# Kernel tuning notes

Measured on AMD Instinct MI355X. Metric: run time of the kernel, lower is better.

## Reference

```python
import jax, jax.numpy as jnp
import numpy as np

B, N, K, D, H, PQ, PV = 2, 2048, 30, 128, 4, 8, 4
INV3C = float(np.sqrt(1.0 / (3 * D)))      # 1/sqrt(3*hidden_dim)
INV3 = float(np.sqrt(1.0 / 3.0))
PT_SCALE = float(np.sqrt(1.0 / (3 * (PQ * 9.0 / 2))))


def _gather(nodes, idx):
    # nodes [B,N,...], idx [B,N,K] -> [B,N,K,...]
    return jax.vmap(lambda n, i: n[i])(nodes, idx)


def _ln(x, w, b, eps=1e-5):
    mu = x.mean(-1, keepdims=True)
    var = x.var(-1, keepdims=True)
    return (x - mu) / jnp.sqrt(var + eps) * w + b


def _forward(h_V, h_E, E_idx, R, t, mask_attend, mask_V,
             Wq, bq, Wkv, bkv, Wqp, bqp, Wkvp, bkvp, Wb, bb_, head_weights,
             Wout, bout, ln0_w, ln0_b, ln1_w, ln1_b, Wm1, bm1, Wm2, bm2):
    q = (h_V @ Wq + bq).reshape(B, N, H, D)                     # [B,N,H,C]
    kv = (h_V @ Wkv + bkv).reshape(B, N, H, 2 * D)
    k_, v_ = kv[..., :D], kv[..., D:]

    def apply_rigid(pts):  # pts [B,N,P,3] -> R @ p + t
        return jnp.einsum('bnxy,bnpy->bnpx', R, pts) + t[:, :, None, :]

    # torch builds points by split-into-3-then-stack along last dim
    qp = h_V @ Wqp + bqp                                        # [B,N,H*PQ*3]
    q_pts = jnp.stack(jnp.split(qp, 3, axis=-1), axis=-1)       # [B,N,H*PQ,3]
    q_pts = apply_rigid(q_pts).reshape(B, N, H, PQ, 3)
    kvp = h_V @ Wkvp + bkvp
    kv_pts = jnp.stack(jnp.split(kvp, 3, axis=-1), axis=-1)
    kv_pts = apply_rigid(kv_pts).reshape(B, N, H, PQ + PV, 3)
    k_pts, v_pts = kv_pts[..., :PQ, :], kv_pts[..., PQ:, :]

    b_bias = h_E @ Wb + bb_                                     # [B,N,K,H]
    k_nb = _gather(k_, E_idx)                                   # [B,N,K,H,C]
    a = jnp.einsum('bnhc,bnkhc->bnkh', q, k_nb) * INV3C
    a = a + INV3 * b_bias

    kp_nb = _gather(k_pts, E_idx)                               # [B,N,K,H,PQ,3]
    diff = q_pts[:, :, None] - kp_nb
    pt_att = jnp.sum(diff * diff, axis=-1)                      # [B,N,K,H,PQ]
    hw = jax.nn.softplus(head_weights)                          # [H]
    pt_att = jnp.sum(PT_SCALE * hw[None, None, None, :, None] * pt_att, axis=-1) * -0.5

    att_mask = 100000.0 * (mask_attend - 1.0)                   # [B,N,K]
    a = a + pt_att + att_mask[..., None]
    a = jax.nn.softmax(a, axis=-2)                              # softmax over neighbors K

    v_nb = _gather(v_, E_idx)
    o = jnp.einsum('bnkh,bnkhc->bnhc', a, v_nb).reshape(B, N, H * D)
    vp_nb = _gather(v_pts, E_idx)                               # [B,N,K,H,PV,3]
    o_pt = jnp.einsum('bnkh,bnkhpx->bnhpx', a, vp_nb)
    # invert_apply: R^T (x - t)
    o_pt = jnp.einsum('bnyx,bnhpy->bnhpx', R, o_pt - t[:, :, None, None, :])
    o_pt_norm = jnp.sqrt(jnp.sum(o_pt ** 2, axis=-1) + 1e-8).reshape(B, N, H * PV)
    o_pt = o_pt.reshape(B, N, H * PV, 3)
    o_pair = jnp.einsum('bnkh,bnkc->bnhc', a, h_E).reshape(B, N, H * D)

    cat = jnp.concatenate([o, o_pt[..., 0], o_pt[..., 1], o_pt[..., 2], o_pt_norm, o_pair], axis=-1)
    s = cat @ Wout + bout

    hv = _ln(h_V + s, ln0_w, ln0_b)
    m = jax.nn.relu(hv @ Wm1 + bm1) @ Wm2 + bm2
    hv = _ln(hv + m, ln1_w, ln1_b)
    return hv * mask_V[..., None]


def setup_inputs() -> dict:
    key = jax.random.key(0)
    ks = jax.random.split(key, 16)

    def dense(k, fi, fo):
        kw, kb = jax.random.split(k)
        s = 1.0 / np.sqrt(fi)
        return (jax.random.uniform(kw, (fi, fo), jnp.float32, -s, s),
                jax.random.uniform(kb, (fo,), jnp.float32, -s, s))

    h_V = jax.random.normal(ks[0], (B, N, D), jnp.float32)
    h_E = jax.random.normal(ks[1], (B, N, K, D), jnp.float32)
    E_idx = jax.random.randint(ks[2], (B, N, K), 0, N)
    Rr = jax.random.normal(ks[3], (B, N, 3, 3), jnp.float32)
    R, _ = jnp.linalg.qr(Rr)  # proper orthonormal frames
    t = jax.random.normal(ks[4], (B, N, 3), jnp.float32)
    mask_attend = jnp.ones((B, N, K), jnp.float32)
    mask_V = jnp.ones((B, N), jnp.float32)

    Wq, bq = dense(ks[5], D, D * H)
    Wkv, bkv = dense(ks[6], D, 2 * D * H)
    Wqp, bqp = dense(ks[7], D, H * PQ * 3)
    Wkvp, bkvp = dense(ks[8], D, H * (PQ + PV) * 3)
    Wb, bb_ = dense(ks[9], D, H)
    head_weights = jnp.full((H,), 0.541324854612918, jnp.float32)
    out_dim = H * (D + D + 4 * PV)
    Wout, bout = dense(ks[10], out_dim, D)
    ln0_w = jnp.ones((D,), jnp.float32); ln0_b = jnp.zeros((D,), jnp.float32)
    ln1_w = jnp.ones((D,), jnp.float32); ln1_b = jnp.zeros((D,), jnp.float32)
    Wm1, bm1 = dense(ks[11], D, 4 * D)
    Wm2, bm2 = dense(ks[12], 4 * D, D)
    return dict(h_V=h_V, h_E=h_E, E_idx=E_idx, R=R, t=t,
                mask_attend=mask_attend, mask_V=mask_V,
                Wq=Wq, bq=bq, Wkv=Wkv, bkv=bkv, Wqp=Wqp, bqp=bqp,
                Wkvp=Wkvp, bkvp=bkvp, Wb=Wb, bb_=bb_, head_weights=head_weights,
                Wout=Wout, bout=bout, ln0_w=ln0_w, ln0_b=ln0_b,
                ln1_w=ln1_w, ln1_b=ln1_b, Wm1=Wm1, bm1=bm1, Wm2=Wm2, bm2=bm2)


def reference(h_V, h_E, E_idx, R, t, mask_attend, mask_V,
              Wq, bq, Wkv, bkv, Wqp, bqp, Wkvp, bkvp, Wb, bb_, head_weights,
              Wout, bout, ln0_w, ln0_b, ln1_w, ln1_b, Wm1, bm1, Wm2, bm2):
    return _forward(h_V, h_E, E_idx, R, t, mask_attend, mask_V,
                    Wq, bq, Wkv, bkv, Wqp, bqp, Wkvp, bkvp, Wb, bb_, head_weights,
                    Wout, bout, ln0_w, ln0_b, ln1_w, ln1_b, Wm1, bm1, Wm2, bm2)
```

## Files before the change

kernel.cpp:

```cpp
#include <hip/hip_runtime.h>
#include <math.h>

#define BB 2
#define NN 2048
#define KK 30
#define DD 128
#define HH 4
#define PQ_ 8
#define PV_ 4
#define TM 16

#define INV3C    0.05103103630798288f
#define INV3     0.5773502691896258f
#define PT_SCALE 0.09622504486493764f

typedef __attribute__((ext_vector_type(8))) short short8;
typedef __attribute__((ext_vector_type(4))) float f32x4;
typedef unsigned short ushort_t;

__device__ __forceinline__ ushort_t f2bf(float f) {
    unsigned u = __float_as_uint(f);
    unsigned r = u + 0x7FFFu + ((u >> 16) & 1u);
    return (ushort_t)(r >> 16);
}
__device__ __forceinline__ float bf2f(ushort_t u) {
    return __uint_as_float(((unsigned)u) << 16);
}
__device__ __forceinline__ float bflo(unsigned u) {
    return __uint_as_float(u << 16);
}
__device__ __forceinline__ float bfhi(unsigned u) {
    return __uint_as_float(u & 0xffff0000u);
}

__global__ __launch_bounds__(256) void prep_kernel(
    const float* __restrict__ Wout, const float* __restrict__ Wm1,
    const float* __restrict__ Wm2,
    const float* __restrict__ Wq, const float* __restrict__ Wkv,
    const float* __restrict__ Wqp, const float* __restrict__ Wkvp,
    ushort_t* __restrict__ WoutT, ushort_t* __restrict__ Wm1T,
    ushort_t* __restrict__ Wm2T, ushort_t* __restrict__ WprojT)
{
    const int stride = gridDim.x * blockDim.x;
    const int t0 = blockIdx.x * blockDim.x + threadIdx.x;
    for (int idx = t0; idx < 128 * 1088; idx += stride) {
        int n = idx / 1088, k = idx - n * 1088;
        WoutT[idx] = f2bf(Wout[(size_t)k * 128 + n]);
    }
    for (int idx = t0; idx < 512 * 128; idx += stride) {
        int n = idx >> 7, k = idx & 127;
        Wm1T[idx] = f2bf(Wm1[(size_t)k * 512 + n]);
    }
    for (int idx = t0; idx < 128 * 512; idx += stride) {
        int n = idx >> 9, k = idx & 511;
        Wm2T[idx] = f2bf(Wm2[(size_t)k * 128 + n]);
    }
    for (int idx = t0; idx < 1792 * 128; idx += stride) {
        int n = idx >> 7, k = idx & 127;
        float v;
        if (n < 512)       v = Wq[(size_t)k * 512 + n];
        else if (n < 1536) v = Wkv[(size_t)k * 1024 + (n - 512)];
        else if (n < 1632) v = Wqp[k * 96 + (n - 1536)];
        else if (n < 1776) v = Wkvp[k * 144 + (n - 1632)];
        else               v = 0.f;
        WprojT[idx] = f2bf(v);
    }
}

__global__ __launch_bounds__(512) void proj_kernel(
    const float* __restrict__ hV, const float* __restrict__ R, const float* __restrict__ tvec,
    const ushort_t* __restrict__ WT,
    const float* __restrict__ bq, const float* __restrict__ bkv,
    const float* __restrict__ bqp, const float* __restrict__ bkvp,
    ushort_t* __restrict__ qb, ushort_t* __restrict__ kb, ushort_t* __restrict__ vb,
    float* __restrict__ qpts, float* __restrict__ kpts, float* __restrict__ vpts)
{
    const int node0 = (blockIdx.x >> 1) * TM;
    const int half  = blockIdx.x & 1;
    const int tid = threadIdx.x;
    const int w = tid >> 6, l = tid & 63, lr = l & 15, lk = l >> 4;

    __shared__ ushort_t s_A[TM][128];
    __shared__ float s_qp[TM][96];
    __shared__ float s_kvp[TM][144];

    {
        int i = tid * 4; int r = i >> 7, c = i & 127;
        float4 x = *(const float4*)&hV[(size_t)(node0 + r) * DD + c];
        s_A[r][c + 0] = f2bf(x.x); s_A[r][c + 1] = f2bf(x.y);
        s_A[r][c + 2] = f2bf(x.z); s_A[r][c + 3] = f2bf(x.w);
    }
    __syncthreads();

    const ushort_t* Ab = &s_A[lr][lk * 8];
    for (int t = 0; t < 7; ++t) {
        const int tile = half * 56 + w * 7 + t;
        const int n = tile * 16 + lr;
        f32x4 acc = {0.f, 0.f, 0.f, 0.f};
        const ushort_t* Bb = WT + (size_t)n * 128 + lk * 8;
        #pragma unroll
        for (int ks = 0; ks < 4; ++ks) {
            short8 a = *(const short8*)(Ab + ks * 32);
            short8 bfr = *(const short8*)(Bb + ks * 32);
            acc = __builtin_amdgcn_mfma_f32_16x16x32_bf16(a, bfr, acc, 0, 0, 0);
        }
        if (n < 512) {
            float bias = bq[n];
            #pragma unroll
            for (int i = 0; i < 4; ++i)
                qb[(size_t)(node0 + lk * 4 + i) * 512 + n] = f2bf(acc[i] + bias);
        } else if (n < 1536) {
            int n2 = n - 512;
            float bias = bkv[n2];
            int hh = n2 >> 8, wcol = n2 & 255;
            ushort_t* base = (wcol < 128) ? kb : vb;
            int off = hh * DD + (wcol & 127);
            #pragma unroll
            for (int i = 0; i < 4; ++i)
                base[(size_t)(node0 + lk * 4 + i) * 512 + off] = f2bf(acc[i] + bias);
        } else if (n < 1632) {
            int c = n - 1536;
            float bias = bqp[c];
            #pragma unroll
            for (int i = 0; i < 4; ++i) s_qp[lk * 4 + i][c] = acc[i] + bias;
        } else if (n < 1776) {
            int c = n - 1632;
            float bias = bkvp[c];
            #pragma unroll
            for (int i = 0; i < 4; ++i) s_kvp[lk * 4 + i][c] = acc[i] + bias;
        }
    }
    __syncthreads();

    if (half == 1) {
        for (int idx = tid; idx < TM * 96; idx += 512) {
            int r = idx / 96, u = idx % 96;
            int j = u / 3, d = u % 3;
            int node = node0 + r;
            float acc = tvec[node * 3 + d];
            #pragma unroll
            for (int y = 0; y < 3; ++y)
                acc = fmaf(R[node * 9 + d * 3 + y], s_qp[r][y * 32 + j], acc);
            qpts[(size_t)node * 96 + j * 3 + d] = acc;
        }
        for (int idx = tid; idx < TM * 144; idx += 512) {
            int r = idx / 144, u = idx % 144;
            int jj = u / 3, d = u % 3;
            int node = node0 + r;
            float acc = tvec[node * 3 + d];
            #pragma unroll
            for (int y = 0; y < 3; ++y)
                acc = fmaf(R[node * 9 + d * 3 + y], s_kvp[r][y * 48 + jj], acc);
            int hh = jj / 12, pp = jj % 12;
            if (pp < PQ_) kpts[(size_t)node * 96 + (hh * PQ_ + pp) * 3 + d] = acc;
            else          vpts[(size_t)node * 48 + (hh * PV_ + (pp - PQ_)) * 3 + d] = acc;
        }
    }
}

__global__ __launch_bounds__(256, 8) void attn_kernel(
    const float* __restrict__ hE, const int* __restrict__ Eidx,
    const float* __restrict__ R, const float* __restrict__ tvec,
    const float* __restrict__ mask_att,
    const float* __restrict__ Wb, const float* __restrict__ bb,
    const float* __restrict__ head_w,
    const ushort_t* __restrict__ qb, const ushort_t* __restrict__ kb,
    const ushort_t* __restrict__ vb,
    const float* __restrict__ qpts, const float* __restrict__ kpts, const float* __restrict__ vpts,
    ushort_t* __restrict__ catb)
{
    const int node = blockIdx.x;
    const int b = node >> 11;
    const int tid = threadIdx.x;
    const int lane = tid & 63;
    const int wv = tid >> 6;

    __shared__ ushort_t s_hEb[KK * DD];
    __shared__ float s_cat[1088];
    __shared__ float s_qp[96];
    __shared__ float s_p[HH][32];
    __shared__ int   s_j[32];
    __shared__ float s_mask[32];
    __shared__ float s_opt[48];

    if (tid < 96) s_qp[tid] = qpts[(size_t)node * 96 + tid];
    if (tid < KK) {
        s_j[tid] = Eidx[(size_t)node * KK + tid];
        s_mask[tid] = 100000.0f * (mask_att[(size_t)node * KK + tid] - 1.0f);
    }
    {
        const float4* src = (const float4*)(hE + (size_t)node * (KK * DD));
        #pragma unroll
        for (int i = 0; i < 4; ++i) {
            const int idx = tid + i * 256;
            if (idx < 960) {
                float4 x = src[idx];
                unsigned lo = ((unsigned)f2bf(x.y) << 16) | (unsigned)f2bf(x.x);
                unsigned hi = ((unsigned)f2bf(x.w) << 16) | (unsigned)f2bf(x.z);
                *(unsigned*)&s_hEb[idx * 4]     = lo;
                *(unsigned*)&s_hEb[idx * 4 + 2] = hi;
            }
        }
    }
    __syncthreads();

    const int h = wv;
    const int l32 = lane & 31;
    const int g = lane >> 5;

    const unsigned qu0 = *(const unsigned*)&qb[(size_t)node * 512 + h * DD + 2 * l32];
    const unsigned qu1 = *(const unsigned*)&qb[(size_t)node * 512 + h * DD + 64 + 2 * l32];
    const float q0 = bflo(qu0), q1 = bfhi(qu0), q2 = bflo(qu1), q3 = bfhi(qu1);
    const float wb0 = Wb[(2 * l32 +  0) * HH + h];
    const float wb1 = Wb[(2 * l32 +  1) * HH + h];
    const float wb2 = Wb[(2 * l32 + 64) * HH + h];
    const float wb3 = Wb[(2 * l32 + 65) * HH + h];
    const float cpt = -0.5f * PT_SCALE * log1pf(expf(head_w[h]));
    const float bbh = INV3 * bb[h];
    const float qpl = (l32 < 24) ? s_qp[h * 24 + l32] : 0.f;

    #pragma unroll
    for (int kx2 = 0; kx2 < KK / 2; ++kx2) {
        const int k = kx2 * 2 + g;
        size_t jb = (size_t)(b * NN + s_j[k]);
        const ushort_t* kr = kb + jb * 512 + h * DD;
        unsigned ku0 = *(const unsigned*)&kr[2 * l32];
        unsigned ku1 = *(const unsigned*)&kr[64 + 2 * l32];
        unsigned eu0 = *(const unsigned*)&s_hEb[k * DD + 2 * l32];
        unsigned eu1 = *(const unsigned*)&s_hEb[k * DD + 64 + 2 * l32];
        float s = q0 * bflo(ku0) + q1 * bfhi(ku0) + q2 * bflo(ku1) + q3 * bfhi(ku1);
        float t = wb0 * bflo(eu0) + wb1 * bfhi(eu0) + wb2 * bflo(eu1) + wb3 * bfhi(eu1);
        float ptc = 0.f;
        if (l32 < 24) {
            float d = qpl - kpts[jb * 96 + h * 24 + l32];
            ptc = d * d;
        }
        float val = INV3C * s + INV3 * t + cpt * ptc;
        #pragma unroll
        for (int off = 16; off; off >>= 1) val += __shfl_down(val, off, 32);
        if (l32 == 0) s_p[h][k] = val + bbh + s_mask[k];
    }
    __syncthreads();

    {
        float v = (lane < KK) ? s_p[h][lane] : -INFINITY;
        float m = v;
        #pragma unroll
        for (int off = 16; off; off >>= 1) m = fmaxf(m, __shfl_down(m, off));
        m = __shfl(m, 0);
        float e = (lane < KK) ? expf(v - m) : 0.f;
        float s = e;
        #pragma unroll
        for (int off = 16; off; off >>= 1) s += __shfl_down(s, off);
        s = __shfl(s, 0);
        if (lane < KK) s_p[h][lane] = e / s;
    }
    __syncthreads();

    {
        const int oh = tid >> 6;
        const int oc0 = (tid & 63) * 2;
        const ushort_t* vrow = vb + oh * DD + oc0;
        float a0 = 0.f, a1 = 0.f, b0 = 0.f, b1 = 0.f;
        #pragma unroll
        for (int kx = 0; kx < KK; ++kx) {
            unsigned pv = *(const unsigned*)(vrow + (size_t)(b * NN + s_j[kx]) * 512);
            unsigned pe = *(const unsigned*)&s_hEb[kx * DD + oc0];
            float p = s_p[oh][kx];
            a0 = fmaf(p, bflo(pv), a0);
            a1 = fmaf(p, bfhi(pv), a1);
            b0 = fmaf(p, bflo(pe), b0);
            b1 = fmaf(p, bfhi(pe), b1);
        }
        s_cat[oh * DD + oc0]           = a0;
        s_cat[oh * DD + oc0 + 1]       = a1;
        s_cat[576 + oh * DD + oc0]     = b0;
        s_cat[576 + oh * DD + oc0 + 1] = b1;
    }
    if (tid < 48) {
        const int oh = (tid / 3) >> 2;
        float acc = 0.f;
        #pragma unroll
        for (int kx = 0; kx < KK; ++kx)
            acc = fmaf(s_p[oh][kx], vpts[(size_t)(b * NN + s_j[kx]) * 48 + tid], acc);
        s_opt[tid] = acc;
    }
    __syncthreads();
    if (tid < 16) {
        int jj = tid;
        float g0 = s_opt[jj * 3 + 0] - tvec[node * 3 + 0];
        float g1 = s_opt[jj * 3 + 1] - tvec[node * 3 + 1];
        float g2 = s_opt[jj * 3 + 2] - tvec[node * 3 + 2];
        float l0 = R[node * 9 + 0] * g0 + R[node * 9 + 3] * g1 + R[node * 9 + 6] * g2;
        float l1 = R[node * 9 + 1] * g0 + R[node * 9 + 4] * g1 + R[node * 9 + 7] * g2;
        float l2 = R[node * 9 + 2] * g0 + R[node * 9 + 5] * g1 + R[node * 9 + 8] * g2;
        s_cat[512 + 0 * 16 + jj] = l0;
        s_cat[512 + 1 * 16 + jj] = l1;
        s_cat[512 + 2 * 16 + jj] = l2;
        s_cat[560 + jj] = sqrtf(l0 * l0 + l1 * l1 + l2 * l2 + 1e-8f);
    }
    __syncthreads();

    for (int i = tid; i < 1088; i += 256)
        catb[(size_t)node * 1088 + i] = f2bf(s_cat[i]);
}

__global__ __launch_bounds__(512) void tail_kernel(
    const float* __restrict__ hV, const float* __restrict__ maskV,
    const ushort_t* __restrict__ catb,
    const ushort_t* __restrict__ WoutT, const float* __restrict__ bout,
    const float* __restrict__ ln0w, const float* __restrict__ ln0b,
    const float* __restrict__ ln1w, const float* __restrict__ ln1b,
    const ushort_t* __restrict__ Wm1T, const float* __restrict__ bm1,
    const ushort_t* __restrict__ Wm2T, const float* __restrict__ bm2,
    float* __restrict__ out)
{
    const int node0 = blockIdx.x * TM;
    const int tid = threadIdx.x;
    const int w  = tid >> 6;
    const int l  = tid & 63;
    const int lr = l & 15;
    const int lk = l >> 4;

    __shared__ float    s_x[TM][DD];
    __shared__ float    s_hv[TM][DD];
    __shared__ ushort_t s_hvb[TM][136];
    __shared__ ushort_t s_m1[TM][520];
    __shared__ float    s_rs[TM][16];
    __shared__ float    s_rq[TM][16];
    __shared__ float    s_stat[TM][2];

    {
        f32x4 acc = {0.f, 0.f, 0.f, 0.f};
        const ushort_t* Ab = catb + (size_t)(node0 + lr) * 1088 + lk * 8;
        const ushort_t* Bb = WoutT + (size_t)(w * 16 + lr) * 1088 + lk * 8;
        #pragma unroll 2
        for (int ks = 0; ks < 34; ++ks) {
            short8 a = *(const short8*)(Ab + ks * 32);
            short8 bfr = *(const short8*)(Bb + ks * 32);
            acc = __builtin_amdgcn_mfma_f32_16x16x32_bf16(a, bfr, acc, 0, 0, 0);
        }
        #pragma unroll
        for (int i = 0; i < 4; ++i)
            s_x[lk * 4 + i][w * 16 + lr] = acc[i];
    }
    __syncthreads();

    if (tid < 256) {
        int r = tid >> 4, sg = tid & 15;
        float ss = 0.f, sq = 0.f;
        #pragma unroll
        for (int j = 0; j < 8; ++j) {
            int cc = sg * 8 + j;
            float x = s_x[r][cc] + bout[cc] + hV[(size_t)(node0 + r) * DD + cc];
            s_x[r][cc] = x;
            ss += x; sq += x * x;
        }
        s_rs[r][sg] = ss; s_rq[r][sg] = sq;
    }
    __syncthreads();
    if (tid < TM) {
        float ss = 0.f, sq = 0.f;
        #pragma unroll
        for (int sg = 0; sg < 16; ++sg) { ss += s_rs[tid][sg]; sq += s_rq[tid][sg]; }
        float mu = ss / 128.f;
        s_stat[tid][0] = mu;
        s_stat[tid][1] = rsqrtf(sq / 128.f - mu * mu + 1e-5f);
    }
    __syncthreads();
    {
        int idx = tid * 4;
        int r = idx >> 7, cc = idx & 127;
        float mu = s_stat[r][0], rstd = s_stat[r][1];
        #pragma unroll
        for (int j = 0; j < 4; ++j) {
            float hvv = (s_x[r][cc + j] - mu) * rstd * ln0w[cc + j] + ln0b[cc + j];
            s_hv[r][cc + j] = hvv;
            s_hvb[r][cc + j] = f2bf(hvv);
        }
    }
    __syncthreads();

    {
        const ushort_t* Ab = &s_hvb[lr][lk * 8];
        #pragma unroll
        for (int t = 0; t < 4; ++t) {
            int n0 = w * 64 + t * 16;
            f32x4 acc = {0.f, 0.f, 0.f, 0.f};
            const ushort_t* Bb = Wm1T + (size_t)(n0 + lr) * 128 + lk * 8;
            #pragma unroll
            for (int ks = 0; ks < 4; ++ks) {
                short8 a = *(const short8*)(Ab + ks * 32);
                short8 bfr = *(const short8*)(Bb + ks * 32);
                acc = __builtin_amdgcn_mfma_f32_16x16x32_bf16(a, bfr, acc, 0, 0, 0);
            }
            int n = n0 + lr;
            float bm = bm1[n];
            #pragma unroll
            for (int i = 0; i < 4; ++i)
                s_m1[lk * 4 + i][n] = f2bf(fmaxf(acc[i] + bm, 0.f));
        }
    }
    __syncthreads();

    {
        f32x4 acc = {0.f, 0.f, 0.f, 0.f};
        const ushort_t* Ab = &s_m1[lr][lk * 8];
        const ushort_t* Bb = Wm2T + (size_t)(w * 16 + lr) * 512 + lk * 8;
        #pragma unroll 4
        for (int ks = 0; ks < 16; ++ks) {
            short8 a = *(const short8*)(Ab + ks * 32);
            short8 bfr = *(const short8*)(Bb + ks * 32);
            acc = __builtin_amdgcn_mfma_f32_16x16x32_bf16(a, bfr, acc, 0, 0, 0);
        }
        #pragma unroll
        for (int i = 0; i < 4; ++i)
            s_x[lk * 4 + i][w * 16 + lr] = acc[i];
    }
    __syncthreads();

    if (tid < 256) {
        int r = tid >> 4, sg = tid & 15;
        float ss = 0.f, sq = 0.f;
        #pragma unroll
        for (int j = 0; j < 8; ++j) {
            int cc = sg * 8 + j;
            float x = s_x[r][cc] + bm2[cc] + s_hv[r][cc];
            s_x[r][cc] = x;
            ss += x; sq += x * x;
        }
        s_rs[r][sg] = ss; s_rq[r][sg] = sq;
    }
    __syncthreads();
    if (tid < TM) {
        float ss = 0.f, sq = 0.f;
        #pragma unroll
        for (int sg = 0; sg < 16; ++sg) { ss += s_rs[tid][sg]; sq += s_rq[tid][sg]; }
        float mu = ss / 128.f;
        s_stat[tid][0] = mu;
        s_stat[tid][1] = rsqrtf(sq / 128.f - mu * mu + 1e-5f);
    }
    __syncthreads();
    {
        int idx = tid * 4;
        int r = idx >> 7, cc = idx & 127;
        float mu = s_stat[r][0], rstd = s_stat[r][1];
        float mk = maskV[node0 + r];
        float4 o;
        o.x = ((s_x[r][cc + 0] - mu) * rstd * ln1w[cc + 0] + ln1b[cc + 0]) * mk;
        o.y = ((s_x[r][cc + 1] - mu) * rstd * ln1w[cc + 1] + ln1b[cc + 1]) * mk;
        o.z = ((s_x[r][cc + 2] - mu) * rstd * ln1w[cc + 2] + ln1b[cc + 2]) * mk;
        o.w = ((s_x[r][cc + 3] - mu) * rstd * ln1w[cc + 3] + ln1b[cc + 3]) * mk;
        *(float4*)&out[(size_t)(node0 + r) * DD + cc] = o;
    }
}

extern "C" void kernel_launch(void* const* d_in, const int* in_sizes, int n_in,
                              void* d_out, int out_size, void* d_ws, size_t ws_size,
                              hipStream_t stream)
{
    const float* hV      = (const float*)d_in[0];
    const float* hE      = (const float*)d_in[1];
    const int*   Eidx    = (const int*)  d_in[2];
    const float* R       = (const float*)d_in[3];
    const float* tvec    = (const float*)d_in[4];
    const float* mask_at = (const float*)d_in[5];
    const float* maskV   = (const float*)d_in[6];
    const float* Wq      = (const float*)d_in[7];
    const float* bq      = (const float*)d_in[8];
    const float* Wkv     = (const float*)d_in[9];
    const float* bkv     = (const float*)d_in[10];
    const float* Wqp     = (const float*)d_in[11];
    const float* bqp     = (const float*)d_in[12];
    const float* Wkvp    = (const float*)d_in[13];
    const float* bkvp    = (const float*)d_in[14];
    const float* Wb      = (const float*)d_in[15];
    const float* bb      = (const float*)d_in[16];
    const float* hw      = (const float*)d_in[17];
    const float* Wout    = (const float*)d_in[18];
    const float* bout    = (const float*)d_in[19];
    const float* ln0w    = (const float*)d_in[20];
    const float* ln0b    = (const float*)d_in[21];
    const float* ln1w    = (const float*)d_in[22];
    const float* ln1b    = (const float*)d_in[23];
    const float* Wm1     = (const float*)d_in[24];
    const float* bm1     = (const float*)d_in[25];
    const float* Wm2     = (const float*)d_in[26];
    const float* bm2     = (const float*)d_in[27];

    const size_t nodes = (size_t)BB * NN;
    ushort_t* qb     = (ushort_t*)d_ws;
    ushort_t* kb     = qb + nodes * 512;
    ushort_t* vb     = kb + nodes * 512;
    ushort_t* catb   = vb + nodes * 512;
    ushort_t* WoutT  = catb + nodes * 1088;
    ushort_t* Wm1T   = WoutT + 128 * 1088;
    ushort_t* Wm2T   = Wm1T + 512 * 128;
    ushort_t* WprojT = Wm2T + 128 * 512;
    float* qpts = (float*)(WprojT + 1792 * 128);
    float* kpts = qpts + nodes * 96;
    float* vpts = kpts + nodes * 96;

    prep_kernel<<<256, 256, 0, stream>>>(Wout, Wm1, Wm2, Wq, Wkv, Wqp, Wkvp,
                                         WoutT, Wm1T, Wm2T, WprojT);

    proj_kernel<<<(int)(nodes / TM) * 2, 512, 0, stream>>>(
        hV, R, tvec, WprojT, bq, bkv, bqp, bkvp,
        qb, kb, vb, qpts, kpts, vpts);

    attn_kernel<<<(int)nodes, 256, 0, stream>>>(
        hE, Eidx, R, tvec, mask_at,
        Wb, bb, hw,
        qb, kb, vb, qpts, kpts, vpts, catb);

    tail_kernel<<<(int)(nodes / TM), 512, 0, stream>>>(
        hV, maskV, catb,
        WoutT, bout, ln0w, ln0b, ln1w, ln1b,
        Wm1T, bm1, Wm2T, bm2, (float*)d_out);
}
```

Measured before the change: 105.0 us.

## Split attention neighbor loops across two wave groups per head with 512-thread blocks

Measured after the change: 115.9 us. 1.1x slower.

```diff
diff --git a/kernel.cpp b/kernel.cpp
--- a/kernel.cpp
+++ b/kernel.cpp
@@ -158,7 +158,7 @@
     }
 }
 
-__global__ __launch_bounds__(256, 8) void attn_kernel(
+__global__ __launch_bounds__(512, 8) void attn_kernel(
     const float* __restrict__ hE, const int* __restrict__ Eidx,
     const float* __restrict__ R, const float* __restrict__ tvec,
     const float* __restrict__ mask_att,
@@ -174,14 +174,17 @@
     const int tid = threadIdx.x;
     const int lane = tid & 63;
     const int wv = tid >> 6;
+    const int h  = wv & 3;
+    const int kh = wv >> 2;
 
     __shared__ ushort_t s_hEb[KK * DD];
     __shared__ float s_cat[1088];
+    __shared__ float s_cat2[1088];
     __shared__ float s_qp[96];
     __shared__ float s_p[HH][32];
     __shared__ int   s_j[32];
     __shared__ float s_mask[32];
-    __shared__ float s_opt[48];
+    __shared__ float s_opt[2][48];
 
     if (tid < 96) s_qp[tid] = qpts[(size_t)node * 96 + tid];
     if (tid < KK) {
@@ -191,8 +194,8 @@
     {
         const float4* src = (const float4*)(hE + (size_t)node * (KK * DD));
         #pragma unroll
-        for (int i = 0; i < 4; ++i) {
-            const int idx = tid + i * 256;
+        for (int i = 0; i < 2; ++i) {
+            const int idx = tid + i * 512;
             if (idx < 960) {
                 float4 x = src[idx];
                 unsigned lo = ((unsigned)f2bf(x.y) << 16) | (unsigned)f2bf(x.x);
@@ -204,7 +207,6 @@
     }
     __syncthreads();
 
-    const int h = wv;
     const int l32 = lane & 31;
     const int g = lane >> 5;
 
@@ -219,30 +221,33 @@
     const float bbh = INV3 * bb[h];
     const float qpl = (l32 < 24) ? s_qp[h * 24 + l32] : 0.f;
 
-    #pragma unroll
-    for (int kx2 = 0; kx2 < KK / 2; ++kx2) {
-        const int k = kx2 * 2 + g;
-        size_t jb = (size_t)(b * NN + s_j[k]);
-        const ushort_t* kr = kb + jb * 512 + h * DD;
-        unsigned ku0 = *(const unsigned*)&kr[2 * l32];
-        unsigned ku1 = *(const unsigned*)&kr[64 + 2 * l32];
-        unsigned eu0 = *(const unsigned*)&s_hEb[k * DD + 2 * l32];
-        unsigned eu1 = *(const unsigned*)&s_hEb[k * DD + 64 + 2 * l32];
-        float s = q0 * bflo(ku0) + q1 * bfhi(ku0) + q2 * bflo(ku1) + q3 * bfhi(ku1);
-        float t = wb0 * bflo(eu0) + wb1 * bfhi(eu0) + wb2 * bflo(eu1) + wb3 * bfhi(eu1);
-        float ptc = 0.f;
-        if (l32 < 24) {
-            float d = qpl - kpts[jb * 96 + h * 24 + l32];
-            ptc = d * d;
-        }
-        float val = INV3C * s + INV3 * t + cpt * ptc;
-        #pragma unroll
-        for (int off = 16; off; off >>= 1) val += __shfl_down(val, off, 32);
-        if (l32 == 0) s_p[h][k] = val + bbh + s_mask[k];
-    }
-    __syncthreads();
-
-    {
+    {
+        const int kx2_lo = kh * 8;
+        const int kx2_hi = (kh == 0) ? 8 : 15;
+        for (int kx2 = kx2_lo; kx2 < kx2_hi; ++kx2) {
+            const int k = kx2 * 2 + g;
+            size_t jb = (size_t)(b * NN + s_j[k]);
+            const ushort_t* kr = kb + jb * 512 + h * DD;
+            unsigned ku0 = *(const unsigned*)&kr[2 * l32];
+            unsigned ku1 = *(const unsigned*)&kr[64 + 2 * l32];
+            unsigned eu0 = *(const unsigned*)&s_hEb[k * DD + 2 * l32];
+            unsigned eu1 = *(const unsigned*)&s_hEb[k * DD + 64 + 2 * l32];
+            float s = q0 * bflo(ku0) + q1 * bfhi(ku0) + q2 * bflo(ku1) + q3 * bfhi(ku1);
+            float t = wb0 * bflo(eu0) + wb1 * bfhi(eu0) + wb2 * bflo(eu1) + wb3 * bfhi(eu1);
+            float ptc = 0.f;
+            if (l32 < 24) {
+                float d = qpl - kpts[jb * 96 + h * 24 + l32];
+                ptc = d * d;
+            }
+            float val = INV3C * s + INV3 * t + cpt * ptc;
+            #pragma unroll
+            for (int off = 16; off; off >>= 1) val += __shfl_down(val, off, 32);
+            if (l32 == 0) s_p[h][k] = val + bbh + s_mask[k];
+        }
+    }
+    __syncthreads();
+
+    if (wv < 4) {
         float v = (lane < KK) ? s_p[h][lane] : -INFINITY;
         float m = v;
         #pragma unroll
@@ -258,39 +263,52 @@
     __syncthreads();
 
     {
-        const int oh = tid >> 6;
-        const int oc0 = (tid & 63) * 2;
-        const ushort_t* vrow = vb + oh * DD + oc0;
+        const int oc0 = lane * 2;
+        float* dst = (kh == 0) ? s_cat : s_cat2;
+        const ushort_t* vrow = vb + h * DD + oc0;
+        const int k0 = kh * 15;
         float a0 = 0.f, a1 = 0.f, b0 = 0.f, b1 = 0.f;
         #pragma unroll
-        for (int kx = 0; kx < KK; ++kx) {
-            unsigned pv = *(const unsigned*)(vrow + (size_t)(b * NN + s_j[kx]) * 512);
-            unsigned pe = *(const unsigned*)&s_hEb[kx * DD + oc0];
-            float p = s_p[oh][kx];
+        for (int kx = 0; kx < 15; ++kx) {
+            const int kk2 = k0 + kx;
+            unsigned pv = *(const unsigned*)(vrow + (size_t)(b * NN + s_j[kk2]) * 512);
+            unsigned pe = *(const unsigned*)&s_hEb[kk2 * DD + oc0];
+            float p = s_p[h][kk2];
             a0 = fmaf(p, bflo(pv), a0);
             a1 = fmaf(p, bfhi(pv), a1);
             b0 = fmaf(p, bflo(pe), b0);
             b1 = fmaf(p, bfhi(pe), b1);
         }
-        s_cat[oh * DD + oc0]           = a0;
-        s_cat[oh * DD + oc0 + 1]       = a1;
-        s_cat[576 + oh * DD + oc0]     = b0;
-        s_cat[576 + oh * DD + oc0 + 1] = b1;
+        dst[h * DD + oc0]           = a0;
+        dst[h * DD + oc0 + 1]       = a1;
+        dst[576 + h * DD + oc0]     = b0;
+        dst[576 + h * DD + oc0 + 1] = b1;
     }
     if (tid < 48) {
         const int oh = (tid / 3) >> 2;
         float acc = 0.f;
         #pragma unroll
-        for (int kx = 0; kx < KK; ++kx)
+        for (int kx = 0; kx < 15; ++kx)
             acc = fmaf(s_p[oh][kx], vpts[(size_t)(b * NN + s_j[kx]) * 48 + tid], acc);
-        s_opt[tid] = acc;
-    }
-    __syncthreads();
+        s_opt[0][tid] = acc;
+    } else if (tid >= 256 && tid < 304) {
+        const int t = tid - 256;
+        const int oh = (t / 3) >> 2;
+        float acc = 0.f;
+        #pragma unroll
+        for (int kx = 15; kx < 30; ++kx)
+            acc = fmaf(s_p[oh][kx], vpts[(size_t)(b * NN + s_j[kx]) * 48 + t], acc);
+        s_opt[1][t] = acc;
+    }
+    __syncthreads();
+
+    s_cat[tid]       += s_cat2[tid];
+    s_cat[576 + tid] += s_cat2[576 + tid];
     if (tid < 16) {
         int jj = tid;
-        float g0 = s_opt[jj * 3 + 0] - tvec[node * 3 + 0];
-        float g1 = s_opt[jj * 3 + 1] - tvec[node * 3 + 1];
-        float g2 = s_opt[jj * 3 + 2] - tvec[node * 3 + 2];
+        float g0 = s_opt[0][jj * 3 + 0] + s_opt[1][jj * 3 + 0] - tvec[node * 3 + 0];
+        float g1 = s_opt[0][jj * 3 + 1] + s_opt[1][jj * 3 + 1] - tvec[node * 3 + 1];
+        float g2 = s_opt[0][jj * 3 + 2] + s_opt[1][jj * 3 + 2] - tvec[node * 3 + 2];
         float l0 = R[node * 9 + 0] * g0 + R[node * 9 + 3] * g1 + R[node * 9 + 6] * g2;
         float l1 = R[node * 9 + 1] * g0 + R[node * 9 + 4] * g1 + R[node * 9 + 7] * g2;
         float l2 = R[node * 9 + 2] * g0 + R[node * 9 + 5] * g1 + R[node * 9 + 8] * g2;
@@ -301,7 +319,7 @@
     }
     __syncthreads();
 
-    for (int i = tid; i < 1088; i += 256)
+    for (int i = tid; i < 1088; i += 512)
         catb[(size_t)node * 1088 + i] = f2bf(s_cat[i]);
 }
 
@@ -508,7 +526,7 @@
         hV, R, tvec, WprojT, bq, bkv, bqp, bkvp,
         qb, kb, vb, qpts, kpts, vpts);
 
-    attn_kernel<<<(int)nodes, 256, 0, stream>>>(
+    attn_kernel<<<(int)nodes, 512, 0, stream>>>(
         hE, Eidx, R, tvec, mask_at,
         Wb, bb, hw,
         qb, kb, vb, qpts, kpts, vpts, catb);
```
